# Kernel tuning notes

Measured on AMD Instinct MI355X. Metric: run time of the kernel, lower is better.

Reference implementation:

```python
import jax, jax.numpy as jnp
import numpy as np

B, T, C, H = 2, 2048, 1024, 16
HD = C // H


def setup_inputs() -> dict:
    key = jax.random.key(0)
    ks = jax.random.split(key, 6)
    x = jax.random.normal(ks[0], (B, T, C), dtype=jnp.float32)
    s = 0.02  # init scale for weights
    Wq = jax.random.normal(ks[1], (H, HD, C), dtype=jnp.float32) * s
    Wk = jax.random.normal(ks[2], (H, HD, C), dtype=jnp.float32) * s
    Wv = jax.random.normal(ks[3], (H, HD, C), dtype=jnp.float32) * s
    Wp = jax.random.normal(ks[4], (C, C), dtype=jnp.float32) * s
    bp = jnp.zeros((C,), dtype=jnp.float32)
    return {"x": x, "Wq": Wq, "Wk": Wk, "Wv": Wv, "Wp": Wp, "bp": bp}


def reference(x, Wq, Wk, Wv, Wp, bp):
    # ALiBi slopes per head: 2^(i * -8 / H)
    slopes = jnp.exp2(jnp.arange(H, dtype=jnp.float32) * (-8.0 / H))
    idx = jnp.arange(T)
    # linear_bias = (i - j) - 2*tril(i - j) == -|i - j|, then scaled by slope
    dist = jnp.abs(idx[:, None] - idx[None, :]).astype(jnp.float32)  # [T,T]
    bias = -slopes[:, None, None] * dist  # [H,T,T]
    causal = idx[:, None] >= idx[None, :]  # tril mask (True = keep)

    # per-head projections (no bias in the Linears)
    q = jnp.einsum('btc,hdc->bhtd', x, Wq)
    k = jnp.einsum('btc,hdc->bhtd', x, Wk)
    v = jnp.einsum('btc,hdc->bhtd', x, Wv)

    # Faithful to torch.einsum('btc,bTc->bTt', q, k): rows = key time, cols = query time.
    logits = jnp.einsum('bhtd,bhTd->bhTt', q, k) + bias[None]  # [B,H,T,T]
    # mask_causal_logits: fill where tril == 0 (no 1/sqrt(d) scaling in alibi head)
    logits = jnp.where(causal[None, None], logits, -jnp.inf)

    weights = jax.nn.softmax(logits, axis=-1)  # softmax over query axis (faithful)

    # Faithful to torch.einsum('btt,btc->btc', w, v): repeated 't' takes the DIAGONAL.
    diag = jnp.diagonal(weights, axis1=2, axis2=3)  # [B,H,T]
    att = diag[..., None] * v  # [B,H,T,HD]

    # concat heads along feature dim in head order, then output proj
    concat = att.transpose(0, 2, 1, 3).reshape(B, T, C)
    out = concat @ Wp.T + bp  # dropout = 0.0 -> identity
    return (out, weights)
```

## Files before the change

### kernel.cpp

```cpp
#include <hip/hip_runtime.h>
#include <hip/hip_bf16.h>
#include <hip/hip_fp16.h>

typedef _Float16 h8 __attribute__((ext_vector_type(8)));
typedef _Float16 h4 __attribute__((ext_vector_type(4)));
typedef float fx4 __attribute__((ext_vector_type(4)));

__device__ __forceinline__ void load_lds16(const void* g, void* l) {
  __builtin_amdgcn_global_load_lds((const __attribute__((address_space(1))) void*)g,
                                   (__attribute__((address_space(3))) void*)l, 16, 0, 0);
}

__global__ __launch_bounds__(256) void cast_all(
    const float* __restrict__ x, const float* __restrict__ Wq,
    const float* __restrict__ Wk, const float* __restrict__ Wv,
    const float* __restrict__ Wp,
    _Float16* __restrict__ xh, _Float16* __restrict__ wqkv,
    _Float16* __restrict__ wph) {
  int g = blockIdx.x * 256 + threadIdx.x;
  const float* src; _Float16* dst;
  if (g < 524288)      { size_t o = (size_t)g * 8;            src = x  + o; dst = xh + o; }
  else if (g < 655360) { size_t o = (size_t)(g - 524288) * 8; src = Wq + o; dst = wqkv + o; }
  else if (g < 786432) { size_t o = (size_t)(g - 655360) * 8; src = Wk + o; dst = wqkv + 1048576 + o; }
  else if (g < 917504) { size_t o = (size_t)(g - 786432) * 8; src = Wv + o; dst = wqkv + 2097152 + o; }
  else                 { size_t o = (size_t)(g - 917504) * 8; src = Wp + o; dst = wph + o; }
  float4 a = *(const float4*)(src);
  float4 b = *(const float4*)(src + 4);
  h8 o;
  o[0]=(_Float16)a.x; o[1]=(_Float16)a.y; o[2]=(_Float16)a.z; o[3]=(_Float16)a.w;
  o[4]=(_Float16)b.x; o[5]=(_Float16)b.y; o[6]=(_Float16)b.z; o[7]=(_Float16)b.w;
  *(h8*)dst = o;
}

template<bool OUT16, bool BIAS>
__global__ __launch_bounds__(256) void gemm_bt(
    const _Float16* __restrict__ A, const _Float16* __restrict__ Bm,
    void* __restrict__ Cv, const float* __restrict__ bias,
    int M, int N, int K) {
  __shared__ _Float16 As[8192];
  __shared__ _Float16 Bs[8192];
  const int tid  = threadIdx.x;
  const int lane = tid & 63, w = tid >> 6;
  const int chunk = (int)gridDim.x >> 3;
  const int bid = ((int)blockIdx.x & 7) * chunk + ((int)blockIdx.x >> 3);
  const int nb = N >> 7;
  const int m0 = (bid / nb) << 7;
  const int n0 = (bid % nb) << 7;
  const int wm = (w >> 1) << 6, wn = (w & 1) << 6;
  fx4 acc[4][4] = {};
  const int fbase = w * 4096 + lane * 16;

  for (int k0 = 0; k0 < K; k0 += 64) {
    __syncthreads();
#pragma unroll
    for (int q = 0; q < 4; ++q) {
      int f = fbase + q * 1024;
      int row = f >> 7;
      int sch = ((f >> 4) & 7) ^ (row & 7);
      const _Float16* gA = A  + (size_t)(m0 + row) * K + k0 + sch * 8;
      const _Float16* gB = Bm + (size_t)(n0 + row) * K + k0 + sch * 8;
      load_lds16(gA, (char*)As + w * 4096 + q * 1024);
      load_lds16(gB, (char*)Bs + w * 4096 + q * 1024);
    }
    __syncthreads();

    h8 af[4][2], bf[4][2];
#pragma unroll
    for (int s4 = 0; s4 < 4; ++s4) {
#pragma unroll
      for (int kk = 0; kk < 2; ++kk) {
        int rowa = wm + s4 * 16 + (lane & 15);
        int cha  = (kk * 4 + (lane >> 4)) ^ (rowa & 7);
        af[s4][kk] = *(const h8*)((const char*)As + rowa * 128 + cha * 16);
        int rowb = wn + s4 * 16 + (lane & 15);
        int chb  = (kk * 4 + (lane >> 4)) ^ (rowb & 7);
        bf[s4][kk] = *(const h8*)((const char*)Bs + rowb * 128 + chb * 16);
      }
    }
#pragma unroll
    for (int ms = 0; ms < 4; ++ms)
#pragma unroll
      for (int ns = 0; ns < 4; ++ns) {
        acc[ms][ns] = __builtin_amdgcn_mfma_f32_16x16x32_f16(af[ms][0], bf[ns][0], acc[ms][ns], 0, 0, 0);
        acc[ms][ns] = __builtin_amdgcn_mfma_f32_16x16x32_f16(af[ms][1], bf[ns][1], acc[ms][ns], 0, 0, 0);
      }
  }

#pragma unroll
  for (int ms = 0; ms < 4; ++ms) {
    int row0 = m0 + wm + ms * 16 + ((lane >> 4) << 2);
#pragma unroll
    for (int ns = 0; ns < 4; ++ns) {
      int col = n0 + wn + ns * 16 + (lane & 15);
      float bv = BIAS ? bias[col] : 0.0f;
#pragma unroll
      for (int e = 0; e < 4; ++e) {
        float v = acc[ms][ns][e] + bv;
        if (OUT16) ((_Float16*)Cv)[(size_t)(row0 + e) * N + col] = (_Float16)v;
        else       ((float*)Cv)[(size_t)(row0 + e) * N + col] = v;
      }
    }
  }
}

__global__ __launch_bounds__(256, 2) void attn_fused(
    const _Float16* __restrict__ qkv, float* __restrict__ wout,
    float* __restrict__ wdiag) {
  __shared__ _Float16 p16[16 * 2064];
  __shared__ float wsum[4 * 16];

  const int n = (blockIdx.x & 7) * 512 + (blockIdx.x >> 3);
  const int bh = n >> 7, it = n & 127;
  const int b = bh >> 4, h = bh & 15;
  const int i0 = it << 4;
  const int tid = threadIdx.x;
  const int lane = tid & 63, w = tid >> 6;
  const int lm = lane & 15, lg = lane >> 4;
  const int d0 = lg << 3;

  const _Float16* kbase = qkv + (size_t)b * 2048 * 3072 + 1024 + h * 64;
  const _Float16* qbase = qkv + (size_t)b * 2048 * 3072 + h * 64;

  h8 kf0 = *(const h8*)(kbase + (size_t)(i0 + lm) * 3072 + d0);
  h8 kf1 = *(const h8*)(kbase + (size_t)(i0 + lm) * 3072 + 32 + d0);

  const float slope = exp2f(-0.5f * (float)h);

  float psum[4] = {0.f, 0.f, 0.f, 0.f};

  h8 qf0 = {}, qf1 = {}, nqf0 = {}, nqf1 = {};
  if (w <= it) {
    const int j = (w << 4) + lm;
    qf0 = *(const h8*)(qbase + (size_t)j * 3072 + d0);
    qf1 = *(const h8*)(qbase + (size_t)j * 3072 + 32 + d0);
  }
  for (int jt = w; jt <= it; jt += 4) {
    if (jt + 4 <= it) {
      const int j2 = ((jt + 4) << 4) + lm;
      nqf0 = *(const h8*)(qbase + (size_t)j2 * 3072 + d0);
      nqf1 = *(const h8*)(qbase + (size_t)j2 * 3072 + 32 + d0);
    }
    const int j = (jt << 4) + lm;
    fx4 acc = {0.f, 0.f, 0.f, 0.f};
    acc = __builtin_amdgcn_mfma_f32_16x16x32_f16(kf0, qf0, acc, 0, 0, 0);
    acc = __builtin_amdgcn_mfma_f32_16x16x32_f16(kf1, qf1, acc, 0, 0, 0);
    const bool diag = (jt == it);
#pragma unroll
    for (int e = 0; e < 4; ++e) {
      const int il = (lg << 2) + e;
      const int i = i0 + il;
      const bool live = (!diag || j <= i);
      float l = acc[e] - slope * (float)(i - j);
      if (live) psum[e] += __expf(l);
      p16[il * 2064 + j] = (_Float16)(live ? l : -60000.f);
    }
    qf0 = nqf0;
    qf1 = nqf1;
  }
#pragma unroll
  for (int e = 0; e < 4; ++e) {
    float v = psum[e];
    v += __shfl_xor(v, 1);
    v += __shfl_xor(v, 2);
    v += __shfl_xor(v, 4);
    v += __shfl_xor(v, 8);
    if (lm == 0) wsum[w * 16 + (lg << 2) + e] = v;
  }
  __syncthreads();

  float* wrow = wout + (size_t)bh * 4194304;
  float* wd = wdiag + bh * 2048;
  const int jl = lane << 2;
#pragma unroll
  for (int q = 0; q < 4; ++q) {
    const int r = (w << 2) + q;
    const int i = i0 + r;
    const float rv = 1.0f / (wsum[r] + wsum[16 + r] + wsum[32 + r] + wsum[48 + r]);
    float* obase = wrow + (size_t)i * 2048;
    const _Float16* prow = &p16[r * 2064];
#pragma unroll
    for (int c = 0; c < 8; ++c) {
      const int jb = (c << 8) + jl;
      fx4 v = {0.f, 0.f, 0.f, 0.f};
      if (jb <= i) {
        h4 pv = *(const h4*)&prow[jb];
#pragma unroll
        for (int e2 = 0; e2 < 4; ++e2) {
          float wv = (jb + e2 <= i) ? __expf((float)pv[e2]) * rv : 0.f;
          v[e2] = wv;
          if (jb + e2 == i) wd[i] = wv;
        }
      }
      __builtin_nontemporal_store(v, (fx4*)(obase + jb));
    }
  }
}

__global__ __launch_bounds__(256) void diag_scale(
    const _Float16* __restrict__ qkv, const float* __restrict__ wdiag,
    _Float16* __restrict__ ch) {
  const int g = blockIdx.x * 256 + threadIdx.x;
  const int c = (g << 3) & 1023;
  const int bt = g >> 7;
  const int hh = c >> 6;
  const int b = bt >> 11, t = bt & 2047;
  const float wv = wdiag[((b << 4) + hh) * 2048 + t];
  h8 v = *(const h8*)(qkv + (size_t)bt * 3072 + 2048 + c);
  h8 o;
#pragma unroll
  for (int e = 0; e < 8; ++e) o[e] = (_Float16)(wv * (float)v[e]);
  *(h8*)(ch + (size_t)bt * 1024 + c) = o;
}

extern "C" void kernel_launch(void* const* d_in, const int* in_sizes, int n_in,
                              void* d_out, int out_size, void* d_ws, size_t ws_size,
                              hipStream_t stream) {
  (void)in_sizes; (void)n_in; (void)out_size; (void)ws_size;
  const float* x  = (const float*)d_in[0];
  const float* Wq = (const float*)d_in[1];
  const float* Wk = (const float*)d_in[2];
  const float* Wv = (const float*)d_in[3];
  const float* Wp = (const float*)d_in[4];
  const float* bp = (const float*)d_in[5];

  char* ws = (char*)d_ws;
  _Float16* xh   = (_Float16*)(ws);
  _Float16* wqkv = (_Float16*)(ws + 8388608);
  _Float16* wph  = (_Float16*)(ws + 14680064);
  _Float16* qkv  = (_Float16*)(ws + 16777216);
  float*    wdg  = (float*)   (ws + 41943040);
  _Float16* ch   = (_Float16*)(ws + 42467328);

  float* out  = (float*)d_out;
  float* wout = out + 4194304;

  cast_all<<<4096, 256, 0, stream>>>(x, Wq, Wk, Wv, Wp, xh, wqkv, wph);
  gemm_bt<true, false><<<32 * 24, 256, 0, stream>>>(xh, wqkv, (void*)qkv, nullptr, 4096, 3072, 1024);
  attn_fused<<<4096, 256, 0, stream>>>(qkv, wout, wdg);
  diag_scale<<<2048, 256, 0, stream>>>(qkv, wdg, ch);
  gemm_bt<false, true><<<32 * 8, 256, 0, stream>>>(ch, wph, (void*)out, bp, 4096, 1024, 1024);
}
```

Measured before the change: 188.4 us.

## Replace QKV projection GEMM with 256x256-tile double-buffered f16 MFMA kernel

Adds a new GEMM kernel for the QKV projection that uses 256x256 output tiles with 512 threads. Tiles are staged via direct global-to-LDS loads with an XOR swizzle and double buffering, and the MFMA phases run at raised wave priority. The larger tile is meant to raise data reuse and cut global traffic compared with the previous 128-tile GEMM. The tradeoff is only 192 blocks on a 256-CU part, which leaves some CUs idle, plus heavy register use for the 8x4 accumulators.

```diff
diff --git a/kernel.cpp b/kernel.cpp
--- a/kernel.cpp
+++ b/kernel.cpp
@@ -103,6 +103,89 @@
   }
 }
 
+__global__ __launch_bounds__(512, 2) void gemm256_f16(
+    const _Float16* __restrict__ A, const _Float16* __restrict__ Bm,
+    _Float16* __restrict__ C, int M, int N, int K) {
+  __shared__ _Float16 lds[2][2][16384];
+  const int tid = threadIdx.x;
+  const int lane = tid & 63, w = tid >> 6;
+  const int nb = N >> 8;
+  const int chunk = (int)gridDim.x >> 3;
+  const int bid = ((int)blockIdx.x & 7) * chunk + ((int)blockIdx.x >> 3);
+  const int m0 = (bid / nb) << 8;
+  const int n0 = (bid % nb) << 8;
+  const int wm = (w >> 2) << 7;
+  const int wn = (w & 3) << 6;
+
+  fx4 acc[8][4] = {};
+  const int nt = K >> 6;
+
+  auto STAGE = [&](int buf, int k0) {
+#pragma unroll
+    for (int q = 0; q < 4; ++q) {
+      const int o = (((q << 3) + w) * 64 + lane) << 4;
+      const int row = o >> 7;
+      const int s = o ^ ((row & 7) << 4);
+      const int kcol = (s & 127) >> 1;
+      load_lds16(A  + (size_t)(m0 + row) * K + k0 + kcol, (char*)&lds[buf][0][0] + o);
+      load_lds16(Bm + (size_t)(n0 + row) * K + k0 + kcol, (char*)&lds[buf][1][0] + o);
+    }
+  };
+
+  STAGE(0, 0);
+  STAGE(1, 64);
+  asm volatile("s_waitcnt vmcnt(8)" ::: "memory");
+  __builtin_amdgcn_s_barrier();
+
+  for (int t = 0; t < nt; ++t) {
+    const int c = t & 1;
+    const char* As = (const char*)&lds[c][0][0];
+    const char* Bs = (const char*)&lds[c][1][0];
+#pragma unroll
+    for (int ph = 0; ph < 4; ++ph) {
+      const int kk = ph >> 1, mh = (ph & 1) << 2;
+      h8 af[4], bf[4];
+      const int kof = (kk << 6) + ((lane >> 4) << 4);
+      const int swz = (lane & 7) << 4;
+#pragma unroll
+      for (int x = 0; x < 4; ++x) {
+        const int rowa = wm + (mh + x) * 16 + (lane & 15);
+        af[x] = *(const h8*)(As + (((rowa << 7) + kof) ^ swz));
+        const int rowb = wn + x * 16 + (lane & 15);
+        bf[x] = *(const h8*)(Bs + (((rowb << 7) + kof) ^ swz));
+      }
+      __builtin_amdgcn_s_setprio(1);
+#pragma unroll
+      for (int x = 0; x < 4; ++x)
+#pragma unroll
+        for (int y = 0; y < 4; ++y)
+          acc[mh + x][y] = __builtin_amdgcn_mfma_f32_16x16x32_f16(af[x], bf[y], acc[mh + x][y], 0, 0, 0);
+      __builtin_amdgcn_s_setprio(0);
+    }
+    asm volatile("s_waitcnt lgkmcnt(0)" ::: "memory");
+    __builtin_amdgcn_s_barrier();
+    if (t + 2 < nt) {
+      STAGE(c, (t + 2) << 6);
+      asm volatile("s_waitcnt vmcnt(8)" ::: "memory");
+    } else {
+      asm volatile("s_waitcnt vmcnt(0)" ::: "memory");
+    }
+    __builtin_amdgcn_s_barrier();
+  }
+
+#pragma unroll
+  for (int ms = 0; ms < 8; ++ms) {
+    const int row0 = m0 + wm + ms * 16 + ((lane >> 4) << 2);
+#pragma unroll
+    for (int ns = 0; ns < 4; ++ns) {
+      const int col = n0 + wn + ns * 16 + (lane & 15);
+#pragma unroll
+      for (int e = 0; e < 4; ++e)
+        C[(size_t)(row0 + e) * N + col] = (_Float16)acc[ms][ns][e];
+    }
+  }
+}
+
 __global__ __launch_bounds__(256, 2) void attn_fused(
     const _Float16* __restrict__ qkv, float* __restrict__ wout,
     float* __restrict__ wdiag) {
@@ -235,7 +318,7 @@
   float* wout = out + 4194304;
 
   cast_all<<<4096, 256, 0, stream>>>(x, Wq, Wk, Wv, Wp, xh, wqkv, wph);
-  gemm_bt<true, false><<<32 * 24, 256, 0, stream>>>(xh, wqkv, (void*)qkv, nullptr, 4096, 3072, 1024);
+  gemm256_f16<<<192, 512, 0, stream>>>(xh, wqkv, qkv, 4096, 3072, 1024);
   attn_fused<<<4096, 256, 0, stream>>>(qkv, wout, wdg);
   diag_scale<<<2048, 256, 0, stream>>>(qkv, wdg, ch);
   gemm_bt<false, true><<<32 * 8, 256, 0, stream>>>(ch, wph, (void*)out, bp, 4096, 1024, 1024);
```

Result: no change. 189.4 us (+0.5%).
